# Optimization experiments

Measured on AMD Instinct MI355X. Metric: run time of the kernel, lower is better.

The kernel has to match this reference:

```python
import jax, jax.numpy as jnp
import numpy as np

B = 8192
D_IN, D1, D2, D3, D_OUT = 784, 256, 1024, 256, 10
N_STEPS = 20
LR_INFER = 0.1
GAMMA = 0.1


def setup_inputs() -> dict:
    key = jax.random.key(0)
    ks = jax.random.split(key, 17)
    inp = {
        "x": jax.random.normal(ks[0], (B, D_IN), dtype=jnp.float32),
        # state inits (original does randn*0.1 inside forward)
        "x1_0": jax.random.normal(ks[1], (B, D1), dtype=jnp.float32) * 0.1,
        "x2_0": jax.random.normal(ks[2], (B, D2), dtype=jnp.float32) * 0.1,
        "x3_0": jax.random.normal(ks[3], (B, D3), dtype=jnp.float32) * 0.1,
        "x4_0": jax.random.normal(ks[4], (B, D_OUT), dtype=jnp.float32) * 0.1,
        # parameters (randn*0.1 per __init__)
        "W1": jax.random.normal(ks[5], (D_IN, D1), dtype=jnp.float32) * 0.1,
        "W2": jax.random.normal(ks[6], (D1, D2), dtype=jnp.float32) * 0.1,
        "W3": jax.random.normal(ks[7], (D2, D3), dtype=jnp.float32) * 0.1,
        "W4": jax.random.normal(ks[8], (D3, D_OUT), dtype=jnp.float32) * 0.1,
        "b1": jnp.zeros((D1,), dtype=jnp.float32),
        "b2": jnp.zeros((D2,), dtype=jnp.float32),
        "b3": jnp.zeros((D3,), dtype=jnp.float32),
        "b4": jnp.zeros((D_OUT,), dtype=jnp.float32),
        "L1": jax.random.normal(ks[9], (D1, D1), dtype=jnp.float32) * 0.1,
        "L2": jax.random.normal(ks[10], (D2, D2), dtype=jnp.float32) * 0.1,
        "L3": jax.random.normal(ks[11], (D3, D3), dtype=jnp.float32) * 0.1,
    }
    return inp


def reference(x, x1_0, x2_0, x3_0, x4_0, W1, W2, W3, W4, b1, b2, b3, b4, L1, L2, L3):
    sig = jax.nn.sigmoid
    # x1_pred depends only on the (constant) input x; compute once.
    x1_pred = sig(x @ W1 + b1)  # [B, D1]

    def step(carry, _):
        x1, x2, x3 = carry
        x3_pred = sig(x2 @ W3 + b3)        # [B, D3]
        x2_pred = sig(x1 @ W2 + b2)        # [B, D2]
        x4_pred = x3 @ W4 + b4             # [B, D_OUT]
        eps4 = x4_pred - x4_0
        eps3 = x3_pred - x3
        eps2 = x2_pred - x2
        eps1 = x1_pred - x1
        x3_grad = -eps3 + eps4 @ W4.T - GAMMA * (x3 @ L3)
        x2_grad = -eps2 + eps3 @ W3.T - GAMMA * (x2 @ L2)
        x1_grad = -eps1 + eps2 @ W2.T - GAMMA * (x1 @ L1)
        return (x1 - LR_INFER * x1_grad,
                x2 - LR_INFER * x2_grad,
                x3 - LR_INFER * x3_grad), None

    (x1, x2, x3), _ = jax.lax.scan(step, (x1_0, x2_0, x3_0), None, length=N_STEPS)
    return x3 @ W4 + b4  # [B, D_OUT]
```

## Files before the change

kernel.cpp:

```cpp
#include <hip/hip_runtime.h>
#include <hip/hip_bf16.h>
#include <cstdint>
#include <cstring>


#define LRC 0.1f

typedef unsigned short u16;
typedef unsigned int u32;
typedef __attribute__((ext_vector_type(4))) float f32x4;
typedef __attribute__((ext_vector_type(8))) __bf16 bf16x8;

__device__ __forceinline__ u16 f2b(float v) {
  __hip_bfloat16 h = __float2bfloat16(v);
  union { __hip_bfloat16 h; u16 u; } c; c.h = h; return c.u;
}
__device__ __forceinline__ float b2f(u16 u) {
  union { u16 u; __hip_bfloat16 h; } c; c.u = u; return __bfloat162float(c.h);
}
__device__ __forceinline__ float sigf(float x) { return 1.0f / (1.0f + expf(-x)); }

__device__ __forceinline__ void gll16(const void* g, void* l) {
  __builtin_amdgcn_global_load_lds((const __attribute__((address_space(1))) u32*)g,
                                   (__attribute__((address_space(3))) u32*)l,
                                   16, 0, 0);
}

struct GemmDesc {
  const u16* A; const u16* Bt;
  const u16* A2; const u16* Bt2;
  const float* bias; const float* master; const float* pred; const float* aux;
  const u16* eprev;
  float* outF; u16* outB;
  int lda, ldb, lda2, ldb2, K, K2, N, tnl, nblocks, epi;
};
struct Descs { GemmDesc d[6]; int nd; };

__global__ __launch_bounds__(256) void k_gemm_multi(Descs P) {
  int bid = blockIdx.x;
  int base = 0, di = 0;
  while (di + 1 < P.nd && bid >= base + P.d[di].nblocks) { base += P.d[di].nblocks; ++di; }
  const GemmDesc& d = P.d[di];
  int t = bid - base;
  int tid = threadIdx.x;

  if (d.epi == 5) {
    int i = t * 256 + tid;
    int m = i / 10, n = i - m * 10;
    if (m < 8192) {
      const float* xr = d.master + (size_t)m * 256;
      float acc = 0.f;
      #pragma unroll 4
      for (int k = 0; k < 256; ++k) acc = fmaf(xr[k], d.pred[k * 10 + n], acc);
      d.outB[(size_t)m * 32 + n] = f2b(acc + d.bias[n] - d.aux[i]);
    }
    return;
  }

  __shared__ u16 ldsA[8192];
  __shared__ u16 ldsB[8192];

  int w = tid >> 6, l = tid & 63;
  int wm = w & 1, wn = w >> 1;
  int lrow = l & 15, kgrp = l >> 4;

  int tnl = d.tnl;
  int j = t >> 3;
  int tm = (t & 7) * (d.nblocks >> (3 + tnl)) + (j >> tnl);
  int tnn = j & ((1 << tnl) - 1);
  int m0 = tm * 128, n0 = tnn * 128;

  f32x4 zero = {0.f, 0.f, 0.f, 0.f};
  f32x4 acc[4][4];
  #pragma unroll
  for (int a = 0; a < 4; ++a)
    #pragma unroll
    for (int b = 0; b < 4; ++b) acc[a][b] = zero;

  int srow = l >> 2;
  int scol = (l & 3) * 8;

  auto run = [&](const u16* A, int lda, const u16* Bt, int ldb, int K) {
    for (int k0 = 0; k0 < K;) {
      int nsub = (K - k0 >= 64) ? 2 : 1;
      for (int i = 0; i < 2 * nsub; ++i) {
        int c = i * 4 + w;
        int ks = c >> 3, rb = c & 7;
        int row = rb * 16 + srow;
        int col = k0 + ks * 32 + scol;
        gll16(A  + (size_t)(m0 + row) * lda + col, &ldsA[c * 512]);
        gll16(Bt + (size_t)(n0 + row) * ldb + col, &ldsB[c * 512]);
      }
      __syncthreads();
      for (int ks = 0; ks < nsub; ++ks) {
        bf16x8 af[4], bfr[4];
        #pragma unroll
        for (int mi = 0; mi < 4; ++mi)
          af[mi] = *(const bf16x8*)&ldsA[ks * 4096 + (wm * 64 + mi * 16 + lrow) * 32 + kgrp * 8];
        #pragma unroll
        for (int ni = 0; ni < 4; ++ni)
          bfr[ni] = *(const bf16x8*)&ldsB[ks * 4096 + (wn * 64 + ni * 16 + lrow) * 32 + kgrp * 8];
        #pragma unroll
        for (int mi = 0; mi < 4; ++mi)
          #pragma unroll
          for (int ni = 0; ni < 4; ++ni)
            acc[mi][ni] = __builtin_amdgcn_mfma_f32_16x16x32_bf16(af[mi], bfr[ni], acc[mi][ni], 0, 0, 0);
      }
      __syncthreads();
      k0 += nsub * 32;
    }
  };

  run(d.A, d.lda, d.Bt, d.ldb, d.K);
  if (d.K2 > 0) run(d.A2, d.lda2, d.Bt2, d.ldb2, d.K2);

  int epi = d.epi;
  #pragma unroll
  for (int mi = 0; mi < 4; ++mi) {
    #pragma unroll
    for (int ni = 0; ni < 4; ++ni) {
      #pragma unroll
      for (int j2 = 0; j2 < 4; ++j2) {
        int row = m0 + wm * 64 + mi * 16 + kgrp * 4 + j2;
        int col = n0 + wn * 64 + ni * 16 + lrow;
        size_t idx = (size_t)row * d.N + col;
        float a = acc[mi][ni][j2];
        if (epi == 1) {
          float s = sigf(a + d.bias[col]);
          d.outB[idx] = f2b(s - d.master[idx]);
        } else if (epi == 2) {
          d.outF[idx] = sigf(a + d.bias[col]);
        } else if (epi == 3) {
          float v = d.outF[idx];
          float nv = v + LRC * (d.pred[idx] - v) - LRC * a;
          d.outF[idx] = nv; d.outB[idx] = f2b(nv);
        } else {
          float v = d.outF[idx];
          float nv = v + LRC * b2f(d.eprev[idx]) - LRC * a;
          d.outF[idx] = nv; d.outB[idx] = f2b(nv);
        }
      }
    }
  }
}

__global__ void k_state_init(const float* __restrict__ src, float* __restrict__ dstF,
                             u16* __restrict__ dstB, int n) {
  int i = blockIdx.x * 256 + threadIdx.x;
  if (i < n) { float v = src[i]; dstF[i] = v; dstB[i] = f2b(v); }
}
__global__ void k_transpose_scale(const float* __restrict__ src, u16* __restrict__ dst,
                                  int R, int C, float scale) {
  int i = blockIdx.x * 256 + threadIdx.x;
  if (i < R * C) { int r = i / C, c = i - r * C; dst[c * R + r] = f2b(scale * src[i]); }
}
__global__ void k_conv_bf(const float* __restrict__ src, u16* __restrict__ dst, int n) {
  int i = blockIdx.x * 256 + threadIdx.x;
  if (i < n) dst[i] = f2b(src[i]);
}
__global__ void k_w4pad(const float* __restrict__ W4, u16* __restrict__ dst) {
  int i = blockIdx.x * 256 + threadIdx.x;
  if (i < 256 * 32) { int n = i >> 5, k = i & 31; dst[i] = (k < 10) ? f2b(W4[n * 10 + k]) : (u16)0; }
}
__global__ void k_zero16(u16* __restrict__ dst, int n) {
  int i = blockIdx.x * 256 + threadIdx.x;
  if (i < n) dst[i] = 0;
}
__global__ void k_xsplit(const float* __restrict__ x, u16* __restrict__ dst) {
  int i = blockIdx.x * 256 + threadIdx.x;
  if (i < 8192 * 1600) {
    int m = i / 1600, c = i - m * 1600;
    u16 o = 0;
    if (c < 784) o = f2b(x[m * 784 + c]);
    else if (c >= 800 && c < 1584) {
      float v = x[m * 784 + (c - 800)];
      float h = b2f(f2b(v));
      o = f2b(v - h);
    }
    dst[i] = o;
  }
}
__global__ void k_w1c(const float* __restrict__ W1, u16* __restrict__ dst) {
  int i = blockIdx.x * 256 + threadIdx.x;
  if (i < 256 * 1600) {
    int n = i / 1600, c = i - n * 1600;
    u16 o = 0;
    if (c < 784) o = f2b(W1[c * 256 + n]);
    else if (c >= 800 && c < 1584) o = f2b(W1[(c - 800) * 256 + n]);
    dst[i] = o;
  }
}
__global__ void k_final(const float* __restrict__ X3, const float* __restrict__ W4,
                        const float* __restrict__ b4, float* __restrict__ out) {
  int i = blockIdx.x * 256 + threadIdx.x;
  if (i < 8192 * 10) {
    int m = i / 10, n = i - m * 10;
    const float* xr = X3 + (size_t)m * 256;
    float acc = 0.f;
    #pragma unroll 4
    for (int k = 0; k < 256; ++k) acc = fmaf(xr[k], W4[k * 10 + n], acc);
    out[i] = acc + b4[n];
  }
}

extern "C" void kernel_launch(void* const* d_in, const int* in_sizes, int n_in,
                              void* d_out, int out_size, void* d_ws, size_t ws_size,
                              hipStream_t stream) {
  const float* x    = (const float*)d_in[0];
  const float* x1_0 = (const float*)d_in[1];
  const float* x2_0 = (const float*)d_in[2];
  const float* x3_0 = (const float*)d_in[3];
  const float* x4_0 = (const float*)d_in[4];
  const float* W1 = (const float*)d_in[5];
  const float* W2 = (const float*)d_in[6];
  const float* W3 = (const float*)d_in[7];
  const float* W4 = (const float*)d_in[8];
  const float* b1 = (const float*)d_in[9];
  const float* b2 = (const float*)d_in[10];
  const float* b3 = (const float*)d_in[11];
  const float* b4 = (const float*)d_in[12];
  const float* L1 = (const float*)d_in[13];
  const float* L2 = (const float*)d_in[14];
  const float* L3 = (const float*)d_in[15];

  if (ws_size < 140558336u) return;
  char* ws = (char*)d_ws;
  float* X1f   = (float*)(ws + 0);
  float* X2f   = (float*)(ws + 8388608);
  float* X3f   = (float*)(ws + 41943040);
  u16*   X1b[2]= { (u16*)(ws + 50331648), (u16*)(ws + 54525952) };
  u16*   X2b[2]= { (u16*)(ws + 58720256), (u16*)(ws + 75497472) };
  u16*   X3b[2]= { (u16*)(ws + 92274688), (u16*)(ws + 96468992) };
  float* P1    = (float*)(ws + 100663296);
  u16*   E2    = (u16*)(ws + 109051904);
  u16*   E3    = (u16*)(ws + 125829120);
  u16*   E4    = (u16*)(ws + 130023424);
  u16*   XS    = (u16*)(ws + 109051904);
  u16*   W2t   = (u16*)(ws + 135266304);
  u16*   W3t   = (u16*)(ws + 135790592);
  u16*   L1t   = (u16*)(ws + 136314880);
  u16*   L2t   = (u16*)(ws + 136445952);
  u16*   L3t   = (u16*)(ws + 138543104);
  u16*   W2b   = (u16*)(ws + 138674176);
  u16*   W3b   = (u16*)(ws + 139198464);
  u16*   W4tp  = (u16*)(ws + 139722752);
  u16*   W1c   = (u16*)(ws + 139739136);

  dim3 blk(256);
  auto G = [](int n) { return dim3((unsigned)((n + 255) / 256)); };

  k_state_init<<<G(8192*256),  blk, 0, stream>>>(x1_0, X1f, X1b[0], 8192*256);
  k_state_init<<<G(8192*1024), blk, 0, stream>>>(x2_0, X2f, X2b[0], 8192*1024);
  k_state_init<<<G(8192*256),  blk, 0, stream>>>(x3_0, X3f, X3b[0], 8192*256);
  k_transpose_scale<<<G(256*1024),  blk, 0, stream>>>(W2, W2t, 256, 1024, 1.0f);
  k_transpose_scale<<<G(1024*256),  blk, 0, stream>>>(W3, W3t, 1024, 256, 1.0f);
  k_transpose_scale<<<G(256*256),   blk, 0, stream>>>(L1, L1t, 256, 256, -0.1f);
  k_transpose_scale<<<G(1024*1024), blk, 0, stream>>>(L2, L2t, 1024, 1024, -0.1f);
  k_transpose_scale<<<G(256*256),   blk, 0, stream>>>(L3, L3t, 256, 256, -0.1f);
  k_conv_bf<<<G(256*1024), blk, 0, stream>>>(W2, W2b, 256*1024);
  k_conv_bf<<<G(1024*256), blk, 0, stream>>>(W3, W3b, 1024*256);
  k_w4pad<<<G(256*32), blk, 0, stream>>>(W4, W4tp);
  k_xsplit<<<G(8192*1600), blk, 0, stream>>>(x, XS);
  k_w1c<<<G(256*1600), blk, 0, stream>>>(W1, W1c);

  auto mkg = [](const u16* A, const u16* Bt, int lda, int ldb, int K, int N,
                int tnl, int nb, int epi) {
    GemmDesc g; memset(&g, 0, sizeof(g));
    g.A = A; g.Bt = Bt; g.lda = lda; g.ldb = ldb; g.K = K; g.N = N;
    g.tnl = tnl; g.nblocks = nb; g.epi = epi;
    return g;
  };

  {
    Descs pp; memset(&pp, 0, sizeof(pp)); pp.nd = 1;
    pp.d[0] = mkg(XS, W1c, 1600, 1600, 1600, 256, 1, 128, 2);
    pp.d[0].bias = b1; pp.d[0].outF = P1;
    k_gemm_multi<<<dim3(128), blk, 0, stream>>>(pp);
  }
  k_zero16<<<G(8192*32), blk, 0, stream>>>(E4, 8192*32);

  for (int s = 0; s < 20; ++s) {
    int p = s & 1, q = p ^ 1;

    Descs ph1; memset(&ph1, 0, sizeof(ph1)); ph1.nd = 3;
    ph1.d[0] = mkg(X2b[p], W3t, 1024, 1024, 1024, 256, 1, 128, 1);
    ph1.d[0].bias = b3; ph1.d[0].master = X3f; ph1.d[0].outB = E3;
    ph1.d[1] = mkg(X1b[p], W2t, 256, 256, 256, 1024, 3, 512, 1);
    ph1.d[1].bias = b2; ph1.d[1].master = X2f; ph1.d[1].outB = E2;
    ph1.d[2] = mkg(nullptr, nullptr, 0, 0, 0, 0, 0, 320, 5);
    ph1.d[2].master = X3f; ph1.d[2].pred = W4; ph1.d[2].bias = b4;
    ph1.d[2].aux = x4_0; ph1.d[2].outB = E4;
    k_gemm_multi<<<dim3(960), blk, 0, stream>>>(ph1);

    Descs ph2; memset(&ph2, 0, sizeof(ph2)); ph2.nd = 3;
    ph2.d[0] = mkg(E3, W3b, 256, 256, 256, 1024, 3, 512, 4);
    ph2.d[0].A2 = X2b[p]; ph2.d[0].Bt2 = L2t; ph2.d[0].lda2 = 1024;
    ph2.d[0].ldb2 = 1024; ph2.d[0].K2 = 1024;
    ph2.d[0].eprev = E2; ph2.d[0].outF = X2f; ph2.d[0].outB = X2b[q];
    ph2.d[1] = mkg(E2, W2b, 1024, 1024, 1024, 256, 1, 128, 3);
    ph2.d[1].A2 = X1b[p]; ph2.d[1].Bt2 = L1t; ph2.d[1].lda2 = 256;
    ph2.d[1].ldb2 = 256; ph2.d[1].K2 = 256;
    ph2.d[1].pred = P1; ph2.d[1].outF = X1f; ph2.d[1].outB = X1b[q];
    ph2.d[2] = mkg(E4, W4tp, 32, 32, 32, 256, 1, 128, 4);
    ph2.d[2].A2 = X3b[p]; ph2.d[2].Bt2 = L3t; ph2.d[2].lda2 = 256;
    ph2.d[2].ldb2 = 256; ph2.d[2].K2 = 256;
    ph2.d[2].eprev = E3; ph2.d[2].outF = X3f; ph2.d[2].outB = X3b[q];
    k_gemm_multi<<<dim3(768), blk, 0, stream>>>(ph2);
  }

  k_final<<<G(81920), blk, 0, stream>>>(X3f, W4, b4, (float*)d_out);
}
```

Before: 2.476 ms.

## Fold W4 error path into precomputed W4·W4ᵀ−γL3 matrix and constant term

Expands the x3 update algebraically: eps4@W4ᵀ equals x3@(W4 W4ᵀ) plus a constant (b4−x4_0)@W4ᵀ. The combined matrix W4W4ᵀ−γL3 and the constant are precomputed once, so each step does a single 256-K GEMM for x3 with a new epilogue. This removes the scalar per-step x4 prediction blocks and the extra K=32 GEMM pass. The cost is an 8 MB fp32 constant read in every epilogue, and W4W4ᵀ is now rounded to bf16.

```diff
diff --git a/kernel.cpp b/kernel.cpp
--- a/kernel.cpp
+++ b/kernel.cpp
@@ -43,19 +43,6 @@
   const GemmDesc& d = P.d[di];
   int t = bid - base;
   int tid = threadIdx.x;
-
-  if (d.epi == 5) {
-    int i = t * 256 + tid;
-    int m = i / 10, n = i - m * 10;
-    if (m < 8192) {
-      const float* xr = d.master + (size_t)m * 256;
-      float acc = 0.f;
-      #pragma unroll 4
-      for (int k = 0; k < 256; ++k) acc = fmaf(xr[k], d.pred[k * 10 + n], acc);
-      d.outB[(size_t)m * 32 + n] = f2b(acc + d.bias[n] - d.aux[i]);
-    }
-    return;
-  }
 
   __shared__ u16 ldsA[8192];
   __shared__ u16 ldsB[8192];
@@ -134,9 +121,13 @@
           float v = d.outF[idx];
           float nv = v + LRC * (d.pred[idx] - v) - LRC * a;
           d.outF[idx] = nv; d.outB[idx] = f2b(nv);
+        } else if (epi == 4) {
+          float v = d.outF[idx];
+          float nv = v + LRC * b2f(d.eprev[idx]) - LRC * a;
+          d.outF[idx] = nv; d.outB[idx] = f2b(nv);
         } else {
           float v = d.outF[idx];
-          float nv = v + LRC * b2f(d.eprev[idx]) - LRC * a;
+          float nv = v + LRC * b2f(d.eprev[idx]) - LRC * (a + d.pred[idx]);
           d.outF[idx] = nv; d.outB[idx] = f2b(nv);
         }
       }
@@ -158,13 +149,27 @@
   int i = blockIdx.x * 256 + threadIdx.x;
   if (i < n) dst[i] = f2b(src[i]);
 }
-__global__ void k_w4pad(const float* __restrict__ W4, u16* __restrict__ dst) {
-  int i = blockIdx.x * 256 + threadIdx.x;
-  if (i < 256 * 32) { int n = i >> 5, k = i & 31; dst[i] = (k < 10) ? f2b(W4[n * 10 + k]) : (u16)0; }
-}
-__global__ void k_zero16(u16* __restrict__ dst, int n) {
-  int i = blockIdx.x * 256 + threadIdx.x;
-  if (i < n) dst[i] = 0;
+__global__ void k_m4g(const float* __restrict__ W4, const float* __restrict__ L3,
+                      u16* __restrict__ dst) {
+  int i = blockIdx.x * 256 + threadIdx.x;
+  if (i < 256 * 256) {
+    int n = i >> 8, k = i & 255;
+    float s = 0.f;
+    #pragma unroll
+    for (int jj = 0; jj < 10; ++jj) s = fmaf(W4[n * 10 + jj], W4[k * 10 + jj], s);
+    dst[i] = f2b(s - 0.1f * L3[k * 256 + n]);
+  }
+}
+__global__ void k_c4(const float* __restrict__ W4, const float* __restrict__ b4,
+                     const float* __restrict__ x40, float* __restrict__ dst) {
+  int i = blockIdx.x * 256 + threadIdx.x;
+  if (i < 8192 * 256) {
+    int m = i >> 8, n = i & 255;
+    float s = 0.f;
+    #pragma unroll
+    for (int jj = 0; jj < 10; ++jj) s = fmaf(b4[jj] - x40[m * 10 + jj], W4[n * 10 + jj], s);
+    dst[i] = s;
+  }
 }
 __global__ void k_xsplit(const float* __restrict__ x, u16* __restrict__ dst) {
   int i = blockIdx.x * 256 + threadIdx.x;
@@ -223,7 +228,7 @@
   const float* L2 = (const float*)d_in[14];
   const float* L3 = (const float*)d_in[15];
 
-  if (ws_size < 140558336u) return;
+  if (ws_size < 143687680u) return;
   char* ws = (char*)d_ws;
   float* X1f   = (float*)(ws + 0);
   float* X2f   = (float*)(ws + 8388608);
@@ -234,17 +239,16 @@
   float* P1    = (float*)(ws + 100663296);
   u16*   E2    = (u16*)(ws + 109051904);
   u16*   E3    = (u16*)(ws + 125829120);
-  u16*   E4    = (u16*)(ws + 130023424);
+  float* C4    = (float*)(ws + 130023424);
   u16*   XS    = (u16*)(ws + 109051904);
-  u16*   W2t   = (u16*)(ws + 135266304);
-  u16*   W3t   = (u16*)(ws + 135790592);
-  u16*   L1t   = (u16*)(ws + 136314880);
-  u16*   L2t   = (u16*)(ws + 136445952);
-  u16*   L3t   = (u16*)(ws + 138543104);
-  u16*   W2b   = (u16*)(ws + 138674176);
-  u16*   W3b   = (u16*)(ws + 139198464);
-  u16*   W4tp  = (u16*)(ws + 139722752);
-  u16*   W1c   = (u16*)(ws + 139739136);
+  u16*   W2t   = (u16*)(ws + 138412032);
+  u16*   W3t   = (u16*)(ws + 138936320);
+  u16*   L1t   = (u16*)(ws + 139460608);
+  u16*   L2t   = (u16*)(ws + 139591680);
+  u16*   M4G   = (u16*)(ws + 141688832);
+  u16*   W2b   = (u16*)(ws + 141819904);
+  u16*   W3b   = (u16*)(ws + 142344192);
+  u16*   W1c   = (u16*)(ws + 142868480);
 
   dim3 blk(256);
   auto G = [](int n) { return dim3((unsigned)((n + 255) / 256)); };
@@ -256,10 +260,9 @@
   k_transpose_scale<<<G(1024*256),  blk, 0, stream>>>(W3, W3t, 1024, 256, 1.0f);
   k_transpose_scale<<<G(256*256),   blk, 0, stream>>>(L1, L1t, 256, 256, -0.1f);
   k_transpose_scale<<<G(1024*1024), blk, 0, stream>>>(L2, L2t, 1024, 1024, -0.1f);
-  k_transpose_scale<<<G(256*256),   blk, 0, stream>>>(L3, L3t, 256, 256, -0.1f);
   k_conv_bf<<<G(256*1024), blk, 0, stream>>>(W2, W2b, 256*1024);
   k_conv_bf<<<G(1024*256), blk, 0, stream>>>(W3, W3b, 1024*256);
-  k_w4pad<<<G(256*32), blk, 0, stream>>>(W4, W4tp);
+  k_m4g<<<G(256*256), blk, 0, stream>>>(W4, L3, M4G);
   k_xsplit<<<G(8192*1600), blk, 0, stream>>>(x, XS);
   k_w1c<<<G(256*1600), blk, 0, stream>>>(W1, W1c);
 
@@ -277,20 +280,17 @@
     pp.d[0].bias = b1; pp.d[0].outF = P1;
     k_gemm_multi<<<dim3(128), blk, 0, stream>>>(pp);
   }
-  k_zero16<<<G(8192*32), blk, 0, stream>>>(E4, 8192*32);
+  k_c4<<<G(8192*256), blk, 0, stream>>>(W4, b4, x4_0, C4);
 
   for (int s = 0; s < 20; ++s) {
     int p = s & 1, q = p ^ 1;
 
-    Descs ph1; memset(&ph1, 0, sizeof(ph1)); ph1.nd = 3;
+    Descs ph1; memset(&ph1, 0, sizeof(ph1)); ph1.nd = 2;
     ph1.d[0] = mkg(X2b[p], W3t, 1024, 1024, 1024, 256, 1, 128, 1);
     ph1.d[0].bias = b3; ph1.d[0].master = X3f; ph1.d[0].outB = E3;
     ph1.d[1] = mkg(X1b[p], W2t, 256, 256, 256, 1024, 3, 512, 1);
     ph1.d[1].bias = b2; ph1.d[1].master = X2f; ph1.d[1].outB = E2;
-    ph1.d[2] = mkg(nullptr, nullptr, 0, 0, 0, 0, 0, 320, 5);
-    ph1.d[2].master = X3f; ph1.d[2].pred = W4; ph1.d[2].bias = b4;
-    ph1.d[2].aux = x4_0; ph1.d[2].outB = E4;
-    k_gemm_multi<<<dim3(960), blk, 0, stream>>>(ph1);
+    k_gemm_multi<<<dim3(640), blk, 0, stream>>>(ph1);
 
     Descs ph2; memset(&ph2, 0, sizeof(ph2)); ph2.nd = 3;
     ph2.d[0] = mkg(E3, W3b, 256, 256, 256, 1024, 3, 512, 4);
@@ -301,10 +301,9 @@
     ph2.d[1].A2 = X1b[p]; ph2.d[1].Bt2 = L1t; ph2.d[1].lda2 = 256;
     ph2.d[1].ldb2 = 256; ph2.d[1].K2 = 256;
     ph2.d[1].pred = P1; ph2.d[1].outF = X1f; ph2.d[1].outB = X1b[q];
-    ph2.d[2] = mkg(E4, W4tp, 32, 32, 32, 256, 1, 128, 4);
-    ph2.d[2].A2 = X3b[p]; ph2.d[2].Bt2 = L3t; ph2.d[2].lda2 = 256;
-    ph2.d[2].ldb2 = 256; ph2.d[2].K2 = 256;
-    ph2.d[2].eprev = E3; ph2.d[2].outF = X3f; ph2.d[2].outB = X3b[q];
+    ph2.d[2] = mkg(X3b[p], M4G, 256, 256, 256, 256, 1, 128, 6);
+    ph2.d[2].eprev = E3; ph2.d[2].pred = C4;
+    ph2.d[2].outF = X3f; ph2.d[2].outB = X3b[q];
     k_gemm_multi<<<dim3(768), blk, 0, stream>>>(ph2);
   }
 
```

New measurement: 2.409 ms. 2.7% less time.
